# Kernel optimization log

Hardware: AMD Instinct MI355X
Metric: run time of the kernel (lower is better)

Reference implementation:

```python
import jax, jax.numpy as jnp
import numpy as np

F_DIM = 64      # feature_size
N_NODES = 64    # node_num
T_LEN = 24      # seq_len
N_HEADS = 8
BATCH = 16
E = F_DIM * N_NODES          # embed_dim = 4096
HD = E // N_HEADS            # head dim = 512


def setup_inputs() -> dict:
    key = jax.random.key(0)
    ks = jax.random.split(key, 5)
    s = 0.02
    return {
        "x": jax.random.normal(ks[0], (BATCH, F_DIM, T_LEN, N_NODES), jnp.float32),
        "Wqkv": jax.random.normal(ks[1], (3 * E, E), jnp.float32) * s,
        "bqkv": jnp.zeros((3 * E,), jnp.float32),
        "Wo": jax.random.normal(ks[2], (E, E), jnp.float32) * s,
        "bo": jnp.zeros((E,), jnp.float32),
        "Wfc": jax.random.normal(ks[3], (F_DIM, F_DIM), jnp.float32) * s,
        "bfc": jnp.zeros((F_DIM,), jnp.float32),
    }


def reference(x, Wqkv, bqkv, Wo, bo, Wfc, bfc):
    # x: [B, F, T, N]. Teacher-forcing branch of the original forward.
    B, T = x.shape[0], T_LEN
    # tokens: permute(2,0,1,3).reshape(T,B,E) -> E index = f*N + n
    xt = jnp.transpose(x, (2, 0, 1, 3)).reshape(T, B, E)  # [T,B,E]
    # in_proj is per-token, so projecting the full sequence once equals
    # the original's per-prefix projections.
    qkv = xt @ Wqkv.T + bqkv                               # [T,B,3E]
    q, k, v = jnp.split(qkv, 3, axis=-1)
    q = q.reshape(T, B, N_HEADS, HD)
    k = k.reshape(T, B, N_HEADS, HD)
    v = v.reshape(T, B, N_HEADS, HD)
    scores = jnp.einsum('qbhd,kbhd->bhqk', q, k) / np.sqrt(HD).astype(x.dtype)
    # NOTE: the original passes a float tril(ones) mask, which torch ADDS to
    # the scores (adds 1.0 on the lower triangle, 0 above). Reproduce exactly.
    tril_add = jnp.tril(jnp.ones((T, T), x.dtype))
    base = scores + tril_add                               # [B,H,T,T]
    # prefix lengths L = t+1 for steps t = 0..T-2
    L = jnp.arange(1, T)                                   # [T-1]
    keymask = jnp.arange(T)[None, :] < L[:, None]          # [T-1, T]
    masked = jnp.where(keymask[:, None, None, None, :], base[None], -jnp.inf)
    w = jax.nn.softmax(masked, axis=-1)                    # [T-1,B,H,T,T]
    ctx = jnp.einsum('tbhqk,kbhd->tbqhd', w, v).reshape(T - 1, B, T, E)
    out = ctx @ Wo.T + bo                                  # [T-1,B,T,E]
    # adaptive avg pool over the L valid query positions of each prefix
    qm = keymask.astype(out.dtype)                         # q < L
    pooled = jnp.einsum('tbqe,tq->tbe', out, qm) / L[:, None, None].astype(out.dtype)
    # torch: [B,E] -> reshape(B*N, F) -> fc -> relu -> reshape(B, F, 1, N)
    pred = jax.nn.relu(pooled.reshape(T - 1, B * N_NODES, F_DIM) @ Wfc.T + bfc)
    preds = pred.reshape(T - 1, B, F_DIM, N_NODES)         # row-major, same as torch
    first = x[:, :, :1, :]                                 # [B,F,1,N]
    rest = jnp.transpose(preds, (1, 2, 0, 3))              # [B,F,T-1,N]
    return jnp.concatenate([first, rest], axis=2)          # [B,F,T,N]
```

## Files before the change

kernel.cpp:

```cpp
#include <hip/hip_runtime.h>
#include <math.h>

#define F_DIM 64
#define N_NODES 64
#define T_LEN 24
#define N_HEADS 8
#define BATCH 16
#define E_DIM 4096
#define HD 512
#define QKV_N 12288
#define MB 384
#define TS 23
#define MP 368
#define MPAD 384

typedef unsigned short ushort_t;
typedef short bf16x8 __attribute__((ext_vector_type(8)));
typedef float f32x4 __attribute__((ext_vector_type(4)));

__device__ inline ushort_t f2bf(float f) {
    return (ushort_t)((__float_as_uint(f) + 0x8000u) >> 16);
}

__device__ inline void async_load16(const ushort_t* g, ushort_t* lds) {
    __builtin_amdgcn_global_load_lds(
        (const __attribute__((address_space(1))) unsigned int*)g,
        (__attribute__((address_space(3))) unsigned int*)lds,
        16, 0, 0);
}

__global__ void k_transpose(const float* __restrict__ x, ushort_t* __restrict__ xt) {
    int m = blockIdx.x;
    int t = m >> 4, b = m & 15;
    const float* xb = x + (size_t)b * (F_DIM * T_LEN * N_NODES) + (size_t)t * N_NODES;
    ushort_t* row = xt + (size_t)m * E_DIM;
    for (int e = threadIdx.x; e < E_DIM; e += 256) {
        int f = e >> 6, n = e & 63;
        row[e] = f2bf(xb[(size_t)f * (T_LEN * N_NODES) + n]);
    }
}

__global__ __launch_bounds__(256, 2) void k_gemm_mfma(
    const ushort_t* __restrict__ A, const float* __restrict__ B,
    float* __restrict__ P, int N, int K, int kc)
{
    __shared__ __align__(16) ushort_t As[3][384 * 32];
    __shared__ __align__(16) ushort_t Bs[2][64 * 32];
    const int tid  = threadIdx.x;
    const int wave = tid >> 6, lane = tid & 63;
    const int lr = lane & 15, lq = lane >> 4;
    const int n0 = blockIdx.x * 64;
    const int kz = blockIdx.z * kc;
    const int nt = kc / 32;

    const int rb = lane >> 2;
    const int cc = ((lane & 3) ^ ((lane >> 3) & 3)) * 8;
    const ushort_t* gA[6];
    int lA[6];
    #pragma unroll
    for (int s = 0; s < 6; ++s) {
        int r = (wave * 6 + s) * 16 + rb;
        gA[s] = A + (size_t)r * K + kz + cc;
        lA[s] = (wave * 6 + s) * 512;
    }

    const int e40 = tid, e41 = tid + 256;
    const int r0 = e40 >> 3, q0 = e40 & 7;
    const int r1 = e41 >> 3, q1 = e41 & 7;
    const float* gB0 = B + (size_t)(n0 + r0) * K + kz + q0 * 4;
    const float* gB1 = B + (size_t)(n0 + r1) * K + kz + q1 * 4;
    const int wb0 = r0 * 64 + (((q0 >> 1) ^ ((r0 >> 1) & 3)) << 4) + ((q0 & 1) << 3);
    const int wb1 = r1 * 64 + (((q1 >> 1) ^ ((r1 >> 1) & 3)) << 4) + ((q1 & 1) << 3);

    const int sw   = ((lq ^ ((lr >> 1) & 3)) << 4);
    const int aoff = (wave * 96 + lr) * 64 + sw;
    const int boff = lr * 64 + sw;

    f32x4 acc[6][4];
    #pragma unroll
    for (int i = 0; i < 6; ++i)
        #pragma unroll
        for (int j = 0; j < 4; ++j)
            acc[i][j] = (f32x4){0.f, 0.f, 0.f, 0.f};

    ushort_t* paR = &As[0][0];
    ushort_t* paN = &As[1][0];
    ushort_t* paW = &As[2][0];

    float4 bA0, bA1, bB0, bB1;

    #pragma unroll
    for (int s = 0; s < 6; ++s) async_load16(gA[s], paR + lA[s]);
    bA0 = *(const float4*)gB0;
    bA1 = *(const float4*)gB1;
    #pragma unroll
    for (int s = 0; s < 6; ++s) async_load16(gA[s] + 32, paN + lA[s]);
    bB0 = *(const float4*)(gB0 + 32);
    bB1 = *(const float4*)(gB1 + 32);

    auto conv8 = [](const float4 v) -> uint2 {
        unsigned x = __float_as_uint(v.x) + 0x8000u;
        unsigned y = __float_as_uint(v.y) + 0x8000u;
        unsigned z = __float_as_uint(v.z) + 0x8000u;
        unsigned w = __float_as_uint(v.w) + 0x8000u;
        return make_uint2(__builtin_amdgcn_perm(y, x, 0x07060302u),
                          __builtin_amdgcn_perm(w, z, 0x07060302u));
    };

    auto compute = [&](const ushort_t* pa, const ushort_t* bsb) {
        bf16x8 bfr[4];
        #pragma unroll
        for (int j = 0; j < 4; ++j)
            bfr[j] = *(const bf16x8*)((const char*)bsb + j * 1024 + boff);
        #pragma unroll
        for (int i = 0; i < 6; ++i) {
            bf16x8 af = *(const bf16x8*)((const char*)pa + i * 1024 + aoff);
            #pragma unroll
            for (int j = 0; j < 4; ++j)
                acc[i][j] = __builtin_amdgcn_mfma_f32_16x16x32_bf16(af, bfr[j], acc[i][j], 0, 0, 0);
        }
    };

    for (int tt = 0; tt < nt; tt += 2) {
        asm volatile("s_waitcnt vmcnt(8)" ::: "memory");
        *(uint2*)((char*)&Bs[0][0] + wb0) = conv8(bA0);
        *(uint2*)((char*)&Bs[0][0] + wb1) = conv8(bA1);
        asm volatile("s_waitcnt lgkmcnt(0)" ::: "memory");
        __builtin_amdgcn_s_barrier();
        __builtin_amdgcn_sched_barrier(0);
        if (tt + 2 < nt) {
            const int ko = (tt + 2) * 32;
            #pragma unroll
            for (int s = 0; s < 6; ++s) async_load16(gA[s] + ko, paW + lA[s]);
            bA0 = *(const float4*)(gB0 + ko);
            bA1 = *(const float4*)(gB1 + ko);
        }
        compute(paR, &Bs[0][0]);
        { ushort_t* tmp = paR; paR = paN; paN = paW; paW = tmp; }

        if (tt + 1 < nt - 1) { asm volatile("s_waitcnt vmcnt(8)" ::: "memory"); }
        else                 { asm volatile("s_waitcnt vmcnt(0)" ::: "memory"); }
        *(uint2*)((char*)&Bs[1][0] + wb0) = conv8(bB0);
        *(uint2*)((char*)&Bs[1][0] + wb1) = conv8(bB1);
        asm volatile("s_waitcnt lgkmcnt(0)" ::: "memory");
        __builtin_amdgcn_s_barrier();
        __builtin_amdgcn_sched_barrier(0);
        if (tt + 3 < nt) {
            const int ko = (tt + 3) * 32;
            #pragma unroll
            for (int s = 0; s < 6; ++s) async_load16(gA[s] + ko, paW + lA[s]);
            bB0 = *(const float4*)(gB0 + ko);
            bB1 = *(const float4*)(gB1 + ko);
        }
        compute(paR, &Bs[1][0]);
        { ushort_t* tmp = paR; paR = paN; paN = paW; paW = tmp; }
    }

    float* Pz = P + (size_t)blockIdx.z * MPAD * N;
    #pragma unroll
    for (int i = 0; i < 6; ++i) {
        int m = wave * 96 + i * 16 + lq * 4;
        #pragma unroll
        for (int r = 0; r < 4; ++r) {
            #pragma unroll
            for (int j = 0; j < 4; ++j)
                Pz[(size_t)(m + r) * N + n0 + j * 16 + lr] = acc[i][j][r];
        }
    }
}

__global__ void k_reduce(const float* __restrict__ P, const float* __restrict__ bias,
                         float* __restrict__ C, int N, int S) {
    int idx = blockIdx.x * 256 + threadIdx.x;
    size_t e = (size_t)idx * 4;
    int n = (int)(e % N);
    float4 a = *(const float4*)(P + e);
    for (int s = 1; s < S; ++s) {
        const float4 b = *(const float4*)(P + (size_t)s * MPAD * N + e);
        a.x += b.x; a.y += b.y; a.z += b.z; a.w += b.w;
    }
    const float4 bb = *(const float4*)(bias + n);
    a.x += bb.x; a.y += bb.y; a.z += bb.z; a.w += bb.w;
    *(float4*)(C + e) = a;
}

__global__ __launch_bounds__(512) void k_attn(const float* __restrict__ qkv,
                                              ushort_t* __restrict__ cbar) {
    int bh = blockIdx.x;
    int b = bh >> 3, h = bh & 7;
    __shared__ float vs[T_LEN * HD];
    __shared__ float ss[T_LEN][25];
    __shared__ float isv[T_LEN][25];
    __shared__ float wbs[TS * T_LEN];
    int tid = threadIdx.x, wave = tid >> 6, lane = tid & 63;
    for (int i4 = tid; i4 < T_LEN * HD / 4; i4 += 512) {
        int t = i4 >> 7, d4 = (i4 & 127) * 4;
        *(float4*)&vs[t * HD + d4] =
            *(const float4*)&qkv[(size_t)(t * BATCH + b) * QKV_N + 2 * E_DIM + h * HD + d4];
    }
    const float scale = 0.044194173824159216f;
    for (int p = wave; p < T_LEN * T_LEN; p += 8) {
        int qi = p / 24, ki = p - qi * 24;
        const float* qp = qkv + (size_t)(qi * BATCH + b) * QKV_N + h * HD + lane * 8;
        const float* kp = qkv + (size_t)(ki * BATCH + b) * QKV_N + E_DIM + h * HD + lane * 8;
        float4 a0 = *(const float4*)qp, a1 = *(const float4*)(qp + 4);
        float4 c0 = *(const float4*)kp, c1 = *(const float4*)(kp + 4);
        float s = a0.x * c0.x + a0.y * c0.y + a0.z * c0.z + a0.w * c0.w
                + a1.x * c1.x + a1.y * c1.y + a1.z * c1.z + a1.w * c1.w;
        #pragma unroll
        for (int off = 32; off > 0; off >>= 1) s += __shfl_xor(s, off);
        if (lane == 0) {
            s *= scale;
            if (ki <= qi) s += 1.f;
            ss[qi][ki] = s;
        }
    }
    __syncthreads();
    if (tid < T_LEN) {
        int q = tid;
        float M = -1e30f;
        for (int k = 0; k < T_LEN; ++k) M = fmaxf(M, ss[q][k]);
        float run = 0.f;
        for (int k = 0; k < T_LEN; ++k) {
            float e = __expf(ss[q][k] - M);
            ss[q][k] = e;
            run += e;
            isv[q][k] = 1.f / run;
        }
    }
    __syncthreads();
    for (int p = tid; p < TS * T_LEN; p += 512) {
        int t = p / 24, k = p - t * 24;
        float w = 0.f;
        if (k <= t) {
            float sum = 0.f;
            for (int q = 0; q <= t; ++q) sum += ss[q][k] * isv[q][t];
            w = sum / (float)(t + 1);
        }
        wbs[p] = w;
    }
    __syncthreads();
    int d = tid;
    for (int t = 0; t < TS; ++t) {
        float a = 0.f;
        #pragma unroll
        for (int k = 0; k < T_LEN; ++k) a += wbs[t * 24 + k] * vs[k * HD + d];
        cbar[(size_t)(t * BATCH + b) * E_DIM + h * HD + d] = f2bf(a);
    }
}

__global__ void k_final(const float* __restrict__ pooled, const float* __restrict__ Wfc,
                        const float* __restrict__ bfc, float* __restrict__ out) {
    int tb = blockIdx.x;
    int t = tb >> 4, b = tb & 15;
    __shared__ float ps[E_DIM];
    __shared__ float wf[64 * 65];
    __shared__ float bf[64];
    int tid = threadIdx.x;
    for (int i = tid; i < E_DIM; i += 256) ps[i] = pooled[(size_t)tb * E_DIM + i];
    for (int i = tid; i < 64 * 64; i += 256) wf[(i >> 6) * 65 + (i & 63)] = Wfc[i];
    if (tid < 64) bf[tid] = bfc[tid];
    __syncthreads();
    for (int p = tid; p < 4096; p += 256) {
        int f = p >> 6, n = p & 63;
        float acc = bf[n];
        #pragma unroll
        for (int g = 0; g < 64; ++g) acc += ps[f * 64 + g] * wf[n * 65 + g];
        out[(size_t)((b * 64 + f) * T_LEN + (t + 1)) * N_NODES + n] = fmaxf(acc, 0.f);
    }
}

__global__ void k_first(const float* __restrict__ x, float* __restrict__ out) {
    int idx = blockIdx.x * 256 + threadIdx.x;
    if (idx >= BATCH * F_DIM * N_NODES) return;
    int b = idx >> 12, f = (idx >> 6) & 63, n = idx & 63;
    size_t o = ((size_t)(b * 64 + f) * T_LEN) * 64 + n;
    out[o] = x[o];
}

extern "C" void kernel_launch(void* const* d_in, const int* in_sizes, int n_in,
                              void* d_out, int out_size, void* d_ws, size_t ws_size,
                              hipStream_t stream) {
    const float* x    = (const float*)d_in[0];
    const float* Wqkv = (const float*)d_in[1];
    const float* bqkv = (const float*)d_in[2];
    const float* Wo   = (const float*)d_in[3];
    const float* bo   = (const float*)d_in[4];
    const float* Wfc  = (const float*)d_in[5];
    const float* bfc  = (const float*)d_in[6];
    float* out = (float*)d_out;

    char* wsb = (char*)d_ws;
    ushort_t* xt   = (ushort_t*)wsb;
    float*    qkv  = (float*)(wsb + 3145728);
    ushort_t* cbar = (ushort_t*)(wsb + 3145728 + 18874368);
    float*  pooled = (float*)(wsb + 3145728 + 18874368 + 3145728);
    size_t base    = 3145728 + 18874368 + 3145728 + 6291456;
    float*  pbuf   = (float*)(wsb + base);

    const size_t pq = (size_t)MPAD * QKV_N * 4;
    const size_t po = (size_t)MPAD * E_DIM * 4;
    int S   = (ws_size >= base + 4 * pq) ? 4 : ((ws_size >= base + 2 * pq) ? 2 : 1);
    int Swo = (ws_size >= base + 8 * po) ? 8 : ((ws_size >= base + 4 * po) ? 4 : 1);

    hipLaunchKernelGGL(k_transpose, dim3(MB), dim3(256), 0, stream, x, xt);

    hipLaunchKernelGGL(k_gemm_mfma, dim3(QKV_N / 64, 1, S), dim3(256), 0, stream,
                       xt, Wqkv, pbuf, QKV_N, E_DIM, E_DIM / S);
    hipLaunchKernelGGL(k_reduce, dim3(MPAD * QKV_N / 4 / 256), dim3(256), 0, stream,
                       pbuf, bqkv, qkv, QKV_N, S);

    hipLaunchKernelGGL(k_attn, dim3(BATCH * N_HEADS), dim3(512), 0, stream, qkv, cbar);

    hipLaunchKernelGGL(k_gemm_mfma, dim3(E_DIM / 64, 1, Swo), dim3(256), 0, stream,
                       cbar, Wo, pbuf, E_DIM, E_DIM, E_DIM / Swo);
    hipLaunchKernelGGL(k_reduce, dim3(MPAD * E_DIM / 4 / 256), dim3(256), 0, stream,
                       pbuf, bo, pooled, E_DIM, Swo);

    hipLaunchKernelGGL(k_final, dim3(TS * BATCH), dim3(256), 0, stream, pooled, Wfc, bfc, out);
    hipLaunchKernelGGL(k_first, dim3((BATCH * F_DIM * N_NODES + 255) / 256), dim3(256), 0, stream, x, out);
}
```

Baseline: 545.9 us.

## Restructure GEMM main loop: register-prefetch fragments, 4-stage B buffer, single barrier

Reworks the split-K MFMA GEMM pipeline. The triple-buffered A tile becomes two A buffers, and the B tile becomes four LDS buffers. All A/B fragments are loaded into registers before the barrier, so the next async loads can overwrite the same buffer, and B is prefetched further ahead with its bf16 conversion deferred. It also adds s_setprio around the MFMA block to favour matrix issue. The intent is fewer waits and barriers per k-step and better overlap of global loads with MFMA, at the cost of more registers and fragile vmcnt bookkeeping.

```diff
diff --git a/kernel.cpp b/kernel.cpp
--- a/kernel.cpp
+++ b/kernel.cpp
@@ -29,6 +29,15 @@
         16, 0, 0);
 }
 
+__device__ inline uint2 conv8(const float4 v) {
+    unsigned x = __float_as_uint(v.x) + 0x8000u;
+    unsigned y = __float_as_uint(v.y) + 0x8000u;
+    unsigned z = __float_as_uint(v.z) + 0x8000u;
+    unsigned w = __float_as_uint(v.w) + 0x8000u;
+    return make_uint2(__builtin_amdgcn_perm(y, x, 0x07060302u),
+                      __builtin_amdgcn_perm(w, z, 0x07060302u));
+}
+
 __global__ void k_transpose(const float* __restrict__ x, ushort_t* __restrict__ xt) {
     int m = blockIdx.x;
     int t = m >> 4, b = m & 15;
@@ -44,8 +53,9 @@
     const ushort_t* __restrict__ A, const float* __restrict__ B,
     float* __restrict__ P, int N, int K, int kc)
 {
-    __shared__ __align__(16) ushort_t As[3][384 * 32];
-    __shared__ __align__(16) ushort_t Bs[2][64 * 32];
+    __shared__ __align__(16) ushort_t As0[384 * 32];
+    __shared__ __align__(16) ushort_t As1[384 * 32];
+    __shared__ __align__(16) ushort_t Bs[4][64 * 32];
     const int tid  = threadIdx.x;
     const int wave = tid >> 6, lane = tid & 63;
     const int lr = lane & 15, lq = lane >> 4;
@@ -83,77 +93,109 @@
         for (int j = 0; j < 4; ++j)
             acc[i][j] = (f32x4){0.f, 0.f, 0.f, 0.f};
 
-    ushort_t* paR = &As[0][0];
-    ushort_t* paN = &As[1][0];
-    ushort_t* paW = &As[2][0];
-
-    float4 bA0, bA1, bB0, bB1;
-
-    #pragma unroll
-    for (int s = 0; s < 6; ++s) async_load16(gA[s], paR + lA[s]);
-    bA0 = *(const float4*)gB0;
-    bA1 = *(const float4*)gB1;
-    #pragma unroll
-    for (int s = 0; s < 6; ++s) async_load16(gA[s] + 32, paN + lA[s]);
-    bB0 = *(const float4*)(gB0 + 32);
-    bB1 = *(const float4*)(gB1 + 32);
-
-    auto conv8 = [](const float4 v) -> uint2 {
-        unsigned x = __float_as_uint(v.x) + 0x8000u;
-        unsigned y = __float_as_uint(v.y) + 0x8000u;
-        unsigned z = __float_as_uint(v.z) + 0x8000u;
-        unsigned w = __float_as_uint(v.w) + 0x8000u;
-        return make_uint2(__builtin_amdgcn_perm(y, x, 0x07060302u),
-                          __builtin_amdgcn_perm(w, z, 0x07060302u));
-    };
-
-    auto compute = [&](const ushort_t* pa, const ushort_t* bsb) {
-        bf16x8 bfr[4];
-        #pragma unroll
-        for (int j = 0; j < 4; ++j)
-            bfr[j] = *(const bf16x8*)((const char*)bsb + j * 1024 + boff);
-        #pragma unroll
-        for (int i = 0; i < 6; ++i) {
-            bf16x8 af = *(const bf16x8*)((const char*)pa + i * 1024 + aoff);
+    float4 bA0 = {0,0,0,0}, bA1 = {0,0,0,0};
+    float4 bB0 = {0,0,0,0}, bB1 = {0,0,0,0};
+    uint2 wE0, wE1, wO0, wO1;
+
+    float4 p00 = *(const float4*)(gB0);
+    float4 p01 = *(const float4*)(gB1);
+    float4 p10 = *(const float4*)(gB0 + 32);
+    float4 p11 = *(const float4*)(gB1 + 32);
+    float4 p20 = *(const float4*)(gB0 + 64);
+    float4 p21 = *(const float4*)(gB1 + 64);
+    float4 p30 = *(const float4*)(gB0 + 96);
+    float4 p31 = *(const float4*)(gB1 + 96);
+    __builtin_amdgcn_sched_barrier(0);
+    #pragma unroll
+    for (int s = 0; s < 6; ++s) async_load16(gA[s], As0 + lA[s]);
+    #pragma unroll
+    for (int s = 0; s < 6; ++s) async_load16(gA[s] + 32, As1 + lA[s]);
+    __builtin_amdgcn_sched_barrier(0);
+    asm volatile("s_waitcnt vmcnt(12)" ::: "memory");
+    *(uint2*)((char*)&Bs[0][0] + wb0) = conv8(p00);
+    *(uint2*)((char*)&Bs[0][0] + wb1) = conv8(p01);
+    *(uint2*)((char*)&Bs[1][0] + wb0) = conv8(p10);
+    *(uint2*)((char*)&Bs[1][0] + wb1) = conv8(p11);
+    *(uint2*)((char*)&Bs[2][0] + wb0) = conv8(p20);
+    *(uint2*)((char*)&Bs[2][0] + wb1) = conv8(p21);
+    *(uint2*)((char*)&Bs[3][0] + wb0) = conv8(p30);
+    *(uint2*)((char*)&Bs[3][0] + wb1) = conv8(p31);
+    asm volatile("s_waitcnt lgkmcnt(0)" ::: "memory");
+    __builtin_amdgcn_s_barrier();
+    __builtin_amdgcn_sched_barrier(0);
+
+    auto mfma_block = [&](bf16x8 (&af)[6], bf16x8 (&bfr)[4]) {
+        __builtin_amdgcn_s_setprio(1);
+        #pragma unroll
+        for (int i = 0; i < 6; ++i)
             #pragma unroll
             for (int j = 0; j < 4; ++j)
-                acc[i][j] = __builtin_amdgcn_mfma_f32_16x16x32_bf16(af, bfr[j], acc[i][j], 0, 0, 0);
-        }
+                acc[i][j] = __builtin_amdgcn_mfma_f32_16x16x32_bf16(af[i], bfr[j], acc[i][j], 0, 0, 0);
+        __builtin_amdgcn_s_setprio(0);
     };
 
-    for (int tt = 0; tt < nt; tt += 2) {
-        asm volatile("s_waitcnt vmcnt(8)" ::: "memory");
-        *(uint2*)((char*)&Bs[0][0] + wb0) = conv8(bA0);
-        *(uint2*)((char*)&Bs[0][0] + wb1) = conv8(bA1);
+    auto step_even = [&](int t, ushort_t* bsr, ushort_t* bsw) {
+        asm volatile("s_waitcnt vmcnt(6)" ::: "memory");
+        wE0 = conv8(bA0); wE1 = conv8(bA1);
+        wO0 = conv8(bB0); wO1 = conv8(bB1);
+        bf16x8 af[6], bfr[4];
+        #pragma unroll
+        for (int j = 0; j < 4; ++j)
+            bfr[j] = *(const bf16x8*)((const char*)bsr + j * 1024 + boff);
+        #pragma unroll
+        for (int i = 0; i < 6; ++i)
+            af[i] = *(const bf16x8*)((const char*)As0 + i * 1024 + aoff);
         asm volatile("s_waitcnt lgkmcnt(0)" ::: "memory");
+        __builtin_amdgcn_sched_barrier(0);
+        if (t + 2 < nt) {
+            const int ko = (t + 2) * 32;
+            #pragma unroll
+            for (int s = 0; s < 6; ++s) async_load16(gA[s] + ko, As0 + lA[s]);
+            const int k4 = (t + 4 < nt) ? (t + 4) * 32 : 0;
+            const int k5 = (t + 5 < nt) ? (t + 5) * 32 : 0;
+            bA0 = *(const float4*)(gB0 + k4); bA1 = *(const float4*)(gB1 + k4);
+            bB0 = *(const float4*)(gB0 + k5); bB1 = *(const float4*)(gB1 + k5);
+        }
         __builtin_amdgcn_s_barrier();
         __builtin_amdgcn_sched_barrier(0);
-        if (tt + 2 < nt) {
-            const int ko = (tt + 2) * 32;
+        if (t >= 2 && t + 2 < nt) {
+            *(uint2*)((char*)bsw + wb0) = wE0;
+            *(uint2*)((char*)bsw + wb1) = wE1;
+        }
+        mfma_block(af, bfr);
+    };
+
+    auto step_odd = [&](int t, ushort_t* bsr, ushort_t* bsw) {
+        if (t == nt - 1) { asm volatile("s_waitcnt vmcnt(0)" ::: "memory"); }
+        else             { asm volatile("s_waitcnt vmcnt(10)" ::: "memory"); }
+        bf16x8 af[6], bfr[4];
+        #pragma unroll
+        for (int j = 0; j < 4; ++j)
+            bfr[j] = *(const bf16x8*)((const char*)bsr + j * 1024 + boff);
+        #pragma unroll
+        for (int i = 0; i < 6; ++i)
+            af[i] = *(const bf16x8*)((const char*)As1 + i * 1024 + aoff);
+        asm volatile("s_waitcnt lgkmcnt(0)" ::: "memory");
+        __builtin_amdgcn_sched_barrier(0);
+        if (t + 2 < nt) {
+            const int ko = (t + 2) * 32;
             #pragma unroll
-            for (int s = 0; s < 6; ++s) async_load16(gA[s] + ko, paW + lA[s]);
-            bA0 = *(const float4*)(gB0 + ko);
-            bA1 = *(const float4*)(gB1 + ko);
-        }
-        compute(paR, &Bs[0][0]);
-        { ushort_t* tmp = paR; paR = paN; paN = paW; paW = tmp; }
-
-        if (tt + 1 < nt - 1) { asm volatile("s_waitcnt vmcnt(8)" ::: "memory"); }
-        else                 { asm volatile("s_waitcnt vmcnt(0)" ::: "memory"); }
-        *(uint2*)((char*)&Bs[1][0] + wb0) = conv8(bB0);
-        *(uint2*)((char*)&Bs[1][0] + wb1) = conv8(bB1);
-        asm volatile("s_waitcnt lgkmcnt(0)" ::: "memory");
+            for (int s = 0; s < 6; ++s) async_load16(gA[s] + ko, As1 + lA[s]);
+        }
         __builtin_amdgcn_s_barrier();
         __builtin_amdgcn_sched_barrier(0);
-        if (tt + 3 < nt) {
-            const int ko = (tt + 3) * 32;
-            #pragma unroll
-            for (int s = 0; s < 6; ++s) async_load16(gA[s] + ko, paW + lA[s]);
-            bB0 = *(const float4*)(gB0 + ko);
-            bB1 = *(const float4*)(gB1 + ko);
-        }
-        compute(paR, &Bs[1][0]);
-        { ushort_t* tmp = paR; paR = paN; paN = paW; paW = tmp; }
+        if (t >= 3 && t + 2 < nt) {
+            *(uint2*)((char*)bsw + wb0) = wO0;
+            *(uint2*)((char*)bsw + wb1) = wO1;
+        }
+        mfma_block(af, bfr);
+    };
+
+    for (int tt = 0; tt < nt; tt += 4) {
+        step_even(tt,     &Bs[0][0], &Bs[2][0]);
+        step_odd (tt + 1, &Bs[1][0], &Bs[3][0]);
+        step_even(tt + 2, &Bs[2][0], &Bs[0][0]);
+        step_odd (tt + 3, &Bs[3][0], &Bs[1][0]);
     }
 
     float* Pz = P + (size_t)blockIdx.z * MPAD * N;
```

Result: faster. 531.0 us (-2.7%).
